# Kernel tuning notes

Measured on AMD Instinct MI355X. Metric: run time of the kernel, lower is better.

## Reference

```python
import jax, jax.numpy as jnp
import numpy as np

EPS = 1e-5
GROUPS = 8


def setup_inputs() -> dict:
    key = jax.random.key(0)
    ks = jax.random.split(key, 7)
    B, C, H, W = 4, 512, 64, 64
    x = jax.random.normal(ks[0], (B, C, H, W), dtype=jnp.float32)
    gn_w = jax.random.normal(ks[1], (C,), dtype=jnp.float32) * 0.02 + 1.0
    gn_b = jax.random.normal(ks[2], (C,), dtype=jnp.float32) * 0.02
    # 1x1 convs stored as [out, in] matrices
    qkv_w = jax.random.normal(ks[3], (3 * C, C), dtype=jnp.float32) * (C ** -0.5)
    qkv_b = jax.random.normal(ks[4], (3 * C,), dtype=jnp.float32) * 0.02
    proj_w = jax.random.normal(ks[5], (C, C), dtype=jnp.float32) * (C ** -0.5)
    proj_b = jax.random.normal(ks[6], (C,), dtype=jnp.float32) * 0.02
    return {"x": x, "gn_w": gn_w, "gn_b": gn_b, "qkv_w": qkv_w,
            "qkv_b": qkv_b, "proj_w": proj_w, "proj_b": proj_b}


def _group_norm(x, w, b):
    B, C, H, W = x.shape
    xg = x.reshape(B, GROUPS, C // GROUPS, H, W)
    mu = jnp.mean(xg, axis=(2, 3, 4), keepdims=True)
    var = jnp.var(xg, axis=(2, 3, 4), keepdims=True)
    xn = ((xg - mu) * jax.lax.rsqrt(var + EPS)).reshape(B, C, H, W)
    return xn * w[None, :, None, None] + b[None, :, None, None]


def reference(x, gn_w, gn_b, qkv_w, qkv_b, proj_w, proj_b):
    B, C, H, W = x.shape
    N = H * W
    scale = C ** (-0.5)
    h = _group_norm(x, gn_w, gn_b)
    # 1x1 conv -> [B, 3C, N]
    qkv = jnp.einsum('oc,bcn->bon', qkv_w, h.reshape(B, C, N)) + qkv_b[None, :, None]
    q, k, v = jnp.split(qkv, 3, axis=1)  # each [B, C, N]
    # scores[b, n, m] = sum_c q[b,c,n] * k[b,c,m]
    attn = jax.nn.softmax(jnp.einsum('bcn,bcm->bnm', q, k) * scale, axis=-1)
    # out[b,c,n] = sum_m v[b,c,m] * attn[b,n,m]   (v @ attn^T)
    hout = jnp.einsum('bcm,bnm->bcn', v, attn)
    proj = jnp.einsum('oc,bcn->bon', proj_w, hout) + proj_b[None, :, None]
    return x + proj.reshape(B, C, H, W)
```

## Files before the change

kernel.cpp:

```cpp
#include <hip/hip_runtime.h>
#include <math.h>

#define SCALE 0.044194173824159216f
#define QI 28.22222222f
#define K8SCL ((4.5f/127.0f)*(4.5f/127.0f)*SCALE)
#define PSCL 0.49609375f
#define VSCL 0.035433070866141736f

typedef __bf16 bf16x8 __attribute__((ext_vector_type(8)));
typedef float  f32x4  __attribute__((ext_vector_type(4)));
typedef int    i32x4  __attribute__((ext_vector_type(4)));
typedef unsigned int u32;

__device__ __forceinline__ void gload16(const void* g, void* l) {
    __builtin_amdgcn_global_load_lds(
        (const __attribute__((address_space(1))) u32*)g,
        (__attribute__((address_space(3))) u32*)l, 16, 0, 0);
}

__global__ __launch_bounds__(256) void gn_part(const float* __restrict__ x,
                                               float* __restrict__ part) {
    int gi = blockIdx.x >> 4, sl = blockIdx.x & 15;
    const float4* p = (const float4*)(x + (size_t)gi * 64 * 4096) + (size_t)sl * 4096;
    float s = 0.f, ss = 0.f;
    #pragma unroll 4
    for (int i = threadIdx.x; i < 4096; i += 256) {
        float4 v = p[i];
        s  += v.x + v.y + v.z + v.w;
        ss += v.x*v.x + v.y*v.y + v.z*v.z + v.w*v.w;
    }
    __shared__ float rs[256], rss[256];
    rs[threadIdx.x] = s; rss[threadIdx.x] = ss;
    __syncthreads();
    for (int o = 128; o > 0; o >>= 1) {
        if (threadIdx.x < o) { rs[threadIdx.x] += rs[threadIdx.x+o]; rss[threadIdx.x] += rss[threadIdx.x+o]; }
        __syncthreads();
    }
    if (threadIdx.x == 0) {
        part[blockIdx.x*2 + 0] = rs[0];
        part[blockIdx.x*2 + 1] = rss[0];
    }
}

__global__ __launch_bounds__(64) void gn_fin(const float* __restrict__ part,
                                             float* __restrict__ stats) {
    int t = threadIdx.x;
    if (t < 32) {
        float s = 0.f, ss = 0.f;
        #pragma unroll
        for (int i = 0; i < 16; ++i) { s += part[(t*16+i)*2]; ss += part[(t*16+i)*2+1]; }
        float inv = 1.0f / (float)(64 * 4096);
        float mu  = s * inv;
        float var = ss * inv - mu * mu;
        stats[t*2 + 0] = mu;
        stats[t*2 + 1] = rsqrtf(var + 1e-5f);
    }
}

__global__ __launch_bounds__(256) void gn_apply_t(const float* __restrict__ x,
                                                  const float* __restrict__ stats,
                                                  const float* __restrict__ gw,
                                                  const float* __restrict__ gb,
                                                  __bf16* __restrict__ hT) {
    __shared__ __bf16 tile[64][88];
    int b = blockIdx.z, c0 = blockIdx.y * 64, n0 = blockIdx.x * 64;
    int t = threadIdx.x;
    float mu  = stats[(b*8 + blockIdx.y)*2];
    float rsg = stats[(b*8 + blockIdx.y)*2 + 1];
    int c = t >> 2, ns = t & 3;
    float a = gw[c0+c] * rsg;
    float d = gb[c0+c] - mu * a;
    const float* xr = x + ((size_t)b*512 + c0 + c)*4096 + n0 + ns*16;
    #pragma unroll
    for (int e4 = 0; e4 < 4; ++e4) {
        float4 v = *(const float4*)(xr + e4*4);
        tile[ns*16 + e4*4 + 0][c] = (__bf16)(v.x*a + d);
        tile[ns*16 + e4*4 + 1][c] = (__bf16)(v.y*a + d);
        tile[ns*16 + e4*4 + 2][c] = (__bf16)(v.z*a + d);
        tile[ns*16 + e4*4 + 3][c] = (__bf16)(v.w*a + d);
    }
    __syncthreads();
    int n = t >> 2, cs = t & 3;
    __bf16* dst = hT + ((size_t)b*4096 + n0 + n)*512 + c0 + cs*16;
    *(uint4*)(dst)     = *(const uint4*)(&tile[n][cs*16]);
    *(uint4*)(dst + 8) = *(const uint4*)(&tile[n][cs*16 + 8]);
}

__global__ __launch_bounds__(256) void wconv2(const float* __restrict__ qw,
                                              const float* __restrict__ pwsrc,
                                              __bf16* __restrict__ dst) {
    int i = (blockIdx.x*256 + threadIdx.x) * 4;
    const float* src = (i < 786432) ? (qw + i) : (pwsrc + (i - 786432));
    float4 v = *(const float4*)src;
    dst[i+0] = (__bf16)v.x; dst[i+1] = (__bf16)v.y;
    dst[i+2] = (__bf16)v.z; dst[i+3] = (__bf16)v.w;
}

template<int MODE>
__global__ __launch_bounds__(256) void mm128(
        const __bf16* __restrict__ A, int lda, size_t sA,
        const __bf16* __restrict__ B, int ldb, size_t sB,
        int Kdim,
        const float* __restrict__ bias,
        const float* __restrict__ res, size_t sR,
        void* __restrict__ out, int ldo, size_t sO) {
    __shared__ __bf16 As[3][128][32];
    __shared__ __bf16 Bs[3][128][32];

    const int t = threadIdx.x, w = t >> 6, l = t & 63;
    const int l15 = l & 15, lq = l >> 4;
    const int bz = blockIdx.z;

    const int gx = gridDim.x;
    int lin = blockIdx.y * gx + blockIdx.x;
    {
        const int nwg = gx * gridDim.y;
        const int qn = nwg >> 3, rn = nwg & 7;
        const int xcd = lin & 7, idx = lin >> 3;
        const int base = (xcd < rn) ? xcd*(qn+1) : rn*(qn+1) + (xcd-rn)*qn;
        lin = base + idx;
    }
    const int j0 = (lin % gx) * 128;
    const int i0 = (lin / gx) * 128;

    const __bf16* Ab = A + sA*bz;
    const __bf16* Bb = B + sB*bz;
    const int rowblk = (w & 1)*64;
    const int colblk = (w >> 1)*64;

    const int slot0 = w*64 + l;
    const int rowS0 = slot0 >> 2;
    const int rowS1 = rowS0 + 64;
    const int csS   = (((slot0 & 3) ^ ((rowS0 >> 1) & 3))) * 8;
    const int off0  = (w*64)*16;
    const int off1  = (256 + w*64)*16;

    f32x4 acc[4][4];
    #pragma unroll
    for (int mr = 0; mr < 4; ++mr)
        #pragma unroll
        for (int nr = 0; nr < 4; ++nr)
            #pragma unroll
            for (int r = 0; r < 4; ++r) acc[mr][nr][r] = 0.f;

    auto STAGE = [&](int kc, int bi) {
        char* Ad = (char*)As[bi];
        char* Bd = (char*)Bs[bi];
        gload16(Ab + (size_t)(i0 + rowS0)*lda + kc + csS, Ad + off0);
        gload16(Ab + (size_t)(i0 + rowS1)*lda + kc + csS, Ad + off1);
        gload16(Bb + (size_t)(j0 + rowS0)*ldb + kc + csS, Bd + off0);
        gload16(Bb + (size_t)(j0 + rowS1)*ldb + kc + csS, Bd + off1);
    };

    const int rsw = (l15 >> 1) & 3;
    const int koff = (lq ^ rsw) << 4;

    const int nch = Kdim >> 5;
    STAGE(0, 0);
    STAGE(32, 1);

    for (int cc = 0; cc < nch; ++cc) {
        if (cc < nch - 1) asm volatile("s_waitcnt vmcnt(4)\n\ts_barrier" ::: "memory");
        else              asm volatile("s_waitcnt vmcnt(0)\n\ts_barrier" ::: "memory");

        const char* Ac = (const char*)As[cc % 3];
        const char* Bc = (const char*)Bs[cc % 3];
        bf16x8 av[4], bv[4];
        #pragma unroll
        for (int mr = 0; mr < 4; ++mr)
            av[mr] = *(const bf16x8*)(Ac + (rowblk + mr*16 + l15)*64 + koff);
        #pragma unroll
        for (int nr = 0; nr < 4; ++nr)
            bv[nr] = *(const bf16x8*)(Bc + (colblk + nr*16 + l15)*64 + koff);
        if (cc + 2 < nch) STAGE((cc + 2)*32, (cc + 2) % 3);
        #pragma unroll
        for (int mr = 0; mr < 4; ++mr)
            #pragma unroll
            for (int nr = 0; nr < 4; ++nr)
                acc[mr][nr] = __builtin_amdgcn_mfma_f32_16x16x32_bf16(av[mr], bv[nr], acc[mr][nr], 0, 0, 0);
    }

    #pragma unroll
    for (int mr = 0; mr < 4; ++mr)
        #pragma unroll
        for (int nr = 0; nr < 4; ++nr) {
            int col = j0 + colblk + nr*16 + l15;
            #pragma unroll
            for (int r = 0; r < 4; ++r) {
                int lrow = rowblk + mr*16 + lq*4 + r;
                int gi = i0 + lrow;
                float v = acc[mr][nr][r];
                if constexpr (MODE == 1) {
                    v += bias[gi];
                    int q = __float2int_rn(v * QI);
                    q = q < -127 ? -127 : (q > 127 ? 127 : q);
                    ((char*)out)[sO*bz + (size_t)gi*ldo + col] = (char)q;
                } else {
                    v += bias[gi] + res[sR*bz + (size_t)gi*ldo + col];
                    ((float*)out)[sO*bz + (size_t)gi*ldo + col] = v;
                }
            }
        }
}

template<int M> struct AccT { using T = f32x4; };
template<> struct AccT<4> { using T = i32x4; };
template<> struct AccT<5> { using T = i32x4; };

#define LDSB (98304 + 4096)
template<int MODE>
__global__ __launch_bounds__(512) void mm256(
        const void* __restrict__ A, int ldaB, size_t sAB,
        const void* __restrict__ B, int ldbB, size_t sBB,
        int Kbytes,
        const float* __restrict__ bias,
        void* __restrict__ out, int ldo, size_t sO,
        float* __restrict__ rowpart) {
    extern __shared__ char smem[];
    char*  Abase = smem;
    char*  Bbase = smem + 49152;
    float* redp  = (float*)(smem + 98304);

    const int t = threadIdx.x, w = t >> 6, l = t & 63;
    const int l15 = l & 15, lq = l >> 4;
    const int bz = (MODE == 4) ? (blockIdx.z >> 1) : blockIdx.z;
    const int kh = (MODE == 4) ? (blockIdx.z & 1) : 0;
    const size_t kbase = (size_t)kh * Kbytes;

    const int gx = gridDim.x;
    int lin = blockIdx.y * gx + blockIdx.x;
    {
        const int nwg = gx * gridDim.y;
        const int qn = nwg >> 3, rn = nwg & 7;
        const int xcd = lin & 7, idx = lin >> 3;
        const int base = (xcd < rn) ? xcd*(qn+1) : rn*(qn+1) + (xcd-rn)*qn;
        lin = base + idx;
    }
    const int j0 = (lin % gx) * 256;
    const int i0 = (lin / gx) * 256;

    const char* Ab = (const char*)A + sAB*bz + kbase;
    const char* Bb = (const char*)B + sBB*bz + kbase;
    const int wr = w & 1;
    const int wc = w >> 1;

    const int slot0 = w*64 + l;
    const int rowS0 = slot0 >> 2;
    const int rowS1 = rowS0 + 128;
    const int csS   = (((slot0 & 3) ^ ((rowS0 >> 1) & 3))) * 16;
    const int off0  = (w*64)*16;
    const int off1  = (512 + w*64)*16;

    typename AccT<MODE>::T acc[8][4];
    #pragma unroll
    for (int mr = 0; mr < 8; ++mr)
        #pragma unroll
        for (int nr = 0; nr < 4; ++nr)
            #pragma unroll
            for (int r = 0; r < 4; ++r) acc[mr][nr][r] = 0;

    auto STAGE = [&](int kc, int bi) {
        char* Ad = Abase + bi*16384;
        char* Bd = Bbase + bi*16384;
        gload16(Ab + (size_t)(i0 + rowS0)*ldaB + kc + csS, Ad + off0);
        gload16(Ab + (size_t)(i0 + rowS1)*ldaB + kc + csS, Ad + off1);
        gload16(Bb + (size_t)(j0 + rowS0)*ldbB + kc + csS, Bd + off0);
        gload16(Bb + (size_t)(j0 + rowS1)*ldbB + kc + csS, Bd + off1);
    };

    const int rsw = (l15 >> 1) & 3;
    const int koff = (lq ^ rsw) << 4;

    const int nch = Kbytes >> 6;
    STAGE(0, 0);
    STAGE(64, 1);

    for (int cc = 0; cc < nch; ++cc) {
        if (cc < nch - 1) asm volatile("s_waitcnt vmcnt(4)\n\ts_barrier" ::: "memory");
        else              asm volatile("s_waitcnt vmcnt(0)\n\ts_barrier" ::: "memory");

        const char* Ac = Abase + (cc % 3)*16384;
        const char* Bc = Bbase + (cc % 3)*16384;
        i32x4 araw[8], braw[4];
        #pragma unroll
        for (int mr = 0; mr < 8; ++mr)
            araw[mr] = *(const i32x4*)(Ac + (wr*128 + mr*16 + l15)*64 + koff);
        #pragma unroll
        for (int nr = 0; nr < 4; ++nr)
            braw[nr] = *(const i32x4*)(Bc + (wc*64 + nr*16 + l15)*64 + koff);
        if (cc + 2 < nch) STAGE((cc + 2)*64, (cc + 2) % 3);
        #pragma unroll
        for (int mr = 0; mr < 8; ++mr)
            #pragma unroll
            for (int nr = 0; nr < 4; ++nr) {
                if constexpr (MODE == 4 || MODE == 5) {
                    acc[mr][nr] = __builtin_amdgcn_mfma_i32_16x16x64_i8(
                        araw[mr], braw[nr], acc[mr][nr], 0, 0, 0);
                } else {
                    acc[mr][nr] = __builtin_amdgcn_mfma_f32_16x16x32_bf16(
                        __builtin_bit_cast(bf16x8, araw[mr]),
                        __builtin_bit_cast(bf16x8, braw[nr]), acc[mr][nr], 0, 0, 0);
                }
            }
    }

    if constexpr (MODE == 5) {
        const int jblk = j0 >> 8;
        float rpart[8][4];
        #pragma unroll
        for (int mr = 0; mr < 8; ++mr)
            #pragma unroll
            for (int r = 0; r < 4; ++r) rpart[mr][r] = 0.f;
        #pragma unroll
        for (int mr = 0; mr < 8; ++mr)
            #pragma unroll
            for (int nr = 0; nr < 4; ++nr) {
                int col = j0 + wc*64 + nr*16 + l15;
                #pragma unroll
                for (int r = 0; r < 4; ++r) {
                    int row = wr*128 + mr*16 + lq*4 + r;
                    float e = __expf((float)acc[mr][nr][r] * K8SCL);
                    int q = __float2int_rn(e * PSCL);
                    if (q > 127) q = 127;
                    ((char*)out)[sO*bz + (size_t)(i0 + row)*ldo + col] = (char)q;
                    rpart[mr][r] += (float)q;
                }
            }
        #pragma unroll
        for (int m = 1; m < 16; m <<= 1)
            #pragma unroll
            for (int mr = 0; mr < 8; ++mr)
                #pragma unroll
                for (int r = 0; r < 4; ++r)
                    rpart[mr][r] += __shfl_xor(rpart[mr][r], m);
        __syncthreads();
        if (l15 == 0) {
            #pragma unroll
            for (int mr = 0; mr < 8; ++mr)
                #pragma unroll
                for (int r = 0; r < 4; ++r)
                    redp[(wr*128 + mr*16 + lq*4 + r)*4 + wc] = rpart[mr][r];
        }
        __syncthreads();
        if (t < 256)
            rowpart[(size_t)bz*131072 + (size_t)jblk*4096 + i0 + t] =
                redp[t*4+0] + redp[t*4+1] + redp[t*4+2] + redp[t*4+3];
        return;
    }

    #pragma unroll
    for (int mr = 0; mr < 8; ++mr)
        #pragma unroll
        for (int nr = 0; nr < 4; ++nr) {
            int col = j0 + wc*64 + nr*16 + l15;
            #pragma unroll
            for (int r = 0; r < 4; ++r) {
                int lrow = wr*128 + mr*16 + lq*4 + r;
                if constexpr (MODE == 0) {
                    float v = (float)acc[mr][nr][r] + bias[col];
                    int q = __float2int_rn(v * QI);
                    q = q < -127 ? -127 : (q > 127 ? 127 : q);
                    char* qk = (char*)out + (size_t)bz*8388608;
                    size_t row = (size_t)(i0 + lrow);
                    char* p = (col < 512) ? (qk + row*512 + col)
                                          : (qk + 2097152 + row*512 + (col - 512));
                    *p = (char)q;
                } else {
                    int* po = (int*)out + sO*bz + (size_t)kh*4096*ldo;
                    po[(size_t)(i0 + lrow)*ldo + col] = acc[mr][nr][r];
                }
            }
        }
}

__global__ __launch_bounds__(256) void pv_reduce(const int* __restrict__ part,
                                                 const float* __restrict__ rowpart,
                                                 __bf16* __restrict__ OT) {
    int b = blockIdx.y, r0 = blockIdx.x * 16;
    __shared__ float rs[16];
    int t = threadIdx.x;
    if (t < 16) {
        const float* rp = rowpart + (size_t)b*131072 + r0 + t;
        float s = 0.f;
        #pragma unroll
        for (int jb = 0; jb < 16; ++jb) s += rp[jb*4096];
        rs[t] = VSCL / s;
    }
    __syncthreads();
    int row = r0 + (t >> 4), cseg = (t & 15) * 32;
    const int* p0 = part + (size_t)b*8388608 + (size_t)row*512 + cseg;
    const int* p1 = p0 + 2097152;
    __bf16* o = OT + (size_t)b*2097152 + (size_t)row*512 + cseg;
    float sc = rs[t >> 4];
    #pragma unroll
    for (int g = 0; g < 4; ++g) {
        int4 a0 = *(const int4*)(p0 + g*8);
        int4 a1 = *(const int4*)(p0 + g*8 + 4);
        int4 b0 = *(const int4*)(p1 + g*8);
        int4 b1 = *(const int4*)(p1 + g*8 + 4);
        bf16x8 r;
        r[0] = (__bf16)((float)(a0.x + b0.x) * sc);
        r[1] = (__bf16)((float)(a0.y + b0.y) * sc);
        r[2] = (__bf16)((float)(a0.z + b0.z) * sc);
        r[3] = (__bf16)((float)(a0.w + b0.w) * sc);
        r[4] = (__bf16)((float)(a1.x + b1.x) * sc);
        r[5] = (__bf16)((float)(a1.y + b1.y) * sc);
        r[6] = (__bf16)((float)(a1.z + b1.z) * sc);
        r[7] = (__bf16)((float)(a1.w + b1.w) * sc);
        *(bf16x8*)(o + g*8) = r;
    }
}

extern "C" void kernel_launch(void* const* d_in, const int* in_sizes, int n_in,
                              void* d_out, int out_size, void* d_ws, size_t ws_size,
                              hipStream_t stream) {
    const float* x      = (const float*)d_in[0];
    const float* gn_w   = (const float*)d_in[1];
    const float* gn_b   = (const float*)d_in[2];
    const float* qkv_w  = (const float*)d_in[3];
    const float* qkv_b  = (const float*)d_in[4];
    const float* proj_w = (const float*)d_in[5];
    const float* proj_b = (const float*)d_in[6];

    char* w8 = (char*)d_ws;
    char*   v8buf = w8 + 33554432;
    __bf16* OT   = (__bf16*)(w8 + 50331648);
    __bf16* wq   = (__bf16*)(w8 + 67108864);
    __bf16* pw   = (__bf16*)(w8 + 68681728);
    float*  rowpart = (float*)(w8 + 69206016);
    float*  part = (float*)(w8 + 71303168);
    float*  st   = (float*)(w8 + 71307264);
    const size_t baseP = 71307520ULL;
    __bf16* hT   = (__bf16*)(w8 + baseP);

    size_t avail = (ws_size > baseP) ? (ws_size - baseP) : 0;
    int cap = (int)(avail / 33554432ULL);
    if (cap < 1) cap = 1;
    if (cap > 4) cap = 4;

    hipFuncSetAttribute((const void*)mm256<0>,
                        hipFuncAttributeMaxDynamicSharedMemorySize, LDSB);
    hipFuncSetAttribute((const void*)mm256<4>,
                        hipFuncAttributeMaxDynamicSharedMemorySize, LDSB);
    hipFuncSetAttribute((const void*)mm256<5>,
                        hipFuncAttributeMaxDynamicSharedMemorySize, LDSB);

    wconv2<<<1024, 256, 0, stream>>>(qkv_w, proj_w, wq);
    gn_part<<<512, 256, 0, stream>>>(x, part);
    gn_fin<<<1, 64, 0, stream>>>(part, st);
    gn_apply_t<<<dim3(64, 8, 4), 256, 0, stream>>>(x, st, gn_w, gn_b, hT);

    mm256<0><<<dim3(4, 16, 4), 512, LDSB, stream>>>(
        hT, 1024, (size_t)4096*1024, wq, 1024, 0, 1024,
        qkv_b, w8, 0, 0, nullptr);
    mm128<1><<<dim3(32, 4, 4), 256, 0, stream>>>(
        wq + (size_t)1024*512, 512, 0, hT, 512, (size_t)4096*512, 512,
        qkv_b + 1024, nullptr, 0, v8buf, 4096, (size_t)512*4096);

    for (int b0 = 0; b0 < 4; b0 += cap) {
        int c = (4 - b0 < cap) ? (4 - b0) : cap;
        char* Pb = w8 + baseP + (size_t)b0*33554432;
        mm256<5><<<dim3(16, 16, c), 512, LDSB, stream>>>(
            w8 + (size_t)b0*8388608, 512, 8388608,
            w8 + (size_t)b0*8388608 + 2097152, 512, 8388608, 512,
            nullptr, Pb, 4096, 33554432,
            rowpart + (size_t)b0*131072);
        mm256<4><<<dim3(2, 16, c*2), 512, LDSB, stream>>>(
            Pb, 4096, 33554432,
            v8buf + (size_t)b0*2097152, 4096, 2097152, 2048,
            nullptr, Pb + 16777216, 512, 8388608,
            nullptr);
        pv_reduce<<<dim3(256, c), 256, 0, stream>>>(
            (const int*)(Pb + 16777216), rowpart + (size_t)b0*131072,
            OT + (size_t)b0*2097152);
    }

    mm128<2><<<dim3(32, 4, 4), 256, 0, stream>>>(
        pw, 512, 0, OT, 512, (size_t)4096*512, 512,
        proj_b, x, (size_t)512*4096, (float*)d_out, 4096, (size_t)512*4096);
}
```

Baseline: 202.9 us.

## Stage GEMM epilogues through LDS, store split-K partials as bf16, fuse weight conversion

The QK-softmax (MODE 5) and QKV (MODE 0) epilogues of the 256-tile GEMM now write quantized int8 results into an LDS tile first. Each row is then written out with 16-byte coalesced stores instead of scattered byte stores. The split-K PV partials are stored as bf16 rather than int32, which halves partial traffic into pv_reduce but rounds large integer accumulators. The weight-conversion kernel is also folded into the GroupNorm partial-sum launch, and exp is rewritten as exp2 with a pre-folded constant.

```diff
diff --git a/kernel.cpp b/kernel.cpp
--- a/kernel.cpp
+++ b/kernel.cpp
@@ -4,6 +4,7 @@
 #define SCALE 0.044194173824159216f
 #define QI 28.22222222f
 #define K8SCL ((4.5f/127.0f)*(4.5f/127.0f)*SCALE)
+#define K8SCL2 (K8SCL * 1.4426950408889634f)
 #define PSCL 0.49609375f
 #define VSCL 0.035433070866141736f
 
@@ -18,8 +19,22 @@
         (__attribute__((address_space(3))) u32*)l, 16, 0, 0);
 }
 
-__global__ __launch_bounds__(256) void gn_part(const float* __restrict__ x,
-                                               float* __restrict__ part) {
+__global__ __launch_bounds__(256) void gn_part_w(const float* __restrict__ x,
+                                                 float* __restrict__ part,
+                                                 const float* __restrict__ qw,
+                                                 const float* __restrict__ pwsrc,
+                                                 __bf16* __restrict__ wdst) {
+    if (blockIdx.x >= 512) {
+        int i = ((blockIdx.x - 512)*256 + threadIdx.x) * 4;
+        #pragma unroll
+        for (int rep = 0; rep < 4; ++rep, i += 262144) {
+            const float* src = (i < 786432) ? (qw + i) : (pwsrc + (i - 786432));
+            float4 v = *(const float4*)src;
+            wdst[i+0] = (__bf16)v.x; wdst[i+1] = (__bf16)v.y;
+            wdst[i+2] = (__bf16)v.z; wdst[i+3] = (__bf16)v.w;
+        }
+        return;
+    }
     int gi = blockIdx.x >> 4, sl = blockIdx.x & 15;
     const float4* p = (const float4*)(x + (size_t)gi * 64 * 4096) + (size_t)sl * 4096;
     float s = 0.f, ss = 0.f;
@@ -86,16 +101,6 @@
     *(uint4*)(dst + 8) = *(const uint4*)(&tile[n][cs*16 + 8]);
 }
 
-__global__ __launch_bounds__(256) void wconv2(const float* __restrict__ qw,
-                                              const float* __restrict__ pwsrc,
-                                              __bf16* __restrict__ dst) {
-    int i = (blockIdx.x*256 + threadIdx.x) * 4;
-    const float* src = (i < 786432) ? (qw + i) : (pwsrc + (i - 786432));
-    float4 v = *(const float4*)src;
-    dst[i+0] = (__bf16)v.x; dst[i+1] = (__bf16)v.y;
-    dst[i+2] = (__bf16)v.z; dst[i+3] = (__bf16)v.w;
-}
-
 template<int MODE>
 __global__ __launch_bounds__(256) void mm128(
         const __bf16* __restrict__ A, int lda, size_t sA,
@@ -220,6 +225,7 @@
     char*  Abase = smem;
     char*  Bbase = smem + 49152;
     float* redp  = (float*)(smem + 98304);
+    char*  ptile = smem;
 
     const int t = threadIdx.x, w = t >> 6, l = t & 63;
     const int l15 = l & 15, lq = l >> 4;
@@ -311,18 +317,19 @@
         for (int mr = 0; mr < 8; ++mr)
             #pragma unroll
             for (int r = 0; r < 4; ++r) rpart[mr][r] = 0.f;
+        __syncthreads();
         #pragma unroll
         for (int mr = 0; mr < 8; ++mr)
             #pragma unroll
             for (int nr = 0; nr < 4; ++nr) {
-                int col = j0 + wc*64 + nr*16 + l15;
+                int colL = wc*64 + nr*16 + l15;
                 #pragma unroll
                 for (int r = 0; r < 4; ++r) {
                     int row = wr*128 + mr*16 + lq*4 + r;
-                    float e = __expf((float)acc[mr][nr][r] * K8SCL);
+                    float e = exp2f((float)acc[mr][nr][r] * K8SCL2);
                     int q = __float2int_rn(e * PSCL);
                     if (q > 127) q = 127;
-                    ((char*)out)[sO*bz + (size_t)(i0 + row)*ldo + col] = (char)q;
+                    ptile[row*272 + colL] = (char)q;
                     rpart[mr][r] += (float)q;
                 }
             }
@@ -333,7 +340,6 @@
                 #pragma unroll
                 for (int r = 0; r < 4; ++r)
                     rpart[mr][r] += __shfl_xor(rpart[mr][r], m);
-        __syncthreads();
         if (l15 == 0) {
             #pragma unroll
             for (int mr = 0; mr < 8; ++mr)
@@ -342,12 +348,50 @@
                     redp[(wr*128 + mr*16 + lq*4 + r)*4 + wc] = rpart[mr][r];
         }
         __syncthreads();
+        {
+            int row = t >> 1, half = t & 1;
+            const char* src = ptile + row*272 + half*128;
+            char* dst = (char*)out + sO*bz + (size_t)(i0 + row)*ldo + j0 + half*128;
+            #pragma unroll
+            for (int i = 0; i < 8; ++i)
+                *(uint4*)(dst + i*16) = *(const uint4*)(src + i*16);
+        }
         if (t < 256)
             rowpart[(size_t)bz*131072 + (size_t)jblk*4096 + i0 + t] =
                 redp[t*4+0] + redp[t*4+1] + redp[t*4+2] + redp[t*4+3];
         return;
     }
 
+    if constexpr (MODE == 0) {
+        __syncthreads();
+        #pragma unroll
+        for (int mr = 0; mr < 8; ++mr)
+            #pragma unroll
+            for (int nr = 0; nr < 4; ++nr) {
+                int colL = wc*64 + nr*16 + l15;
+                float b = bias[j0 + colL];
+                #pragma unroll
+                for (int r = 0; r < 4; ++r) {
+                    int row = wr*128 + mr*16 + lq*4 + r;
+                    float v = (float)acc[mr][nr][r] + b;
+                    int q = __float2int_rn(v * QI);
+                    q = q < -127 ? -127 : (q > 127 ? 127 : q);
+                    ptile[row*272 + colL] = (char)q;
+                }
+            }
+        __syncthreads();
+        int row = t >> 1, half = t & 1;
+        int colg = j0 + half*128;
+        const char* src = ptile + row*272 + half*128;
+        char* qk = (char*)out + (size_t)bz*8388608;
+        char* dst = (colg < 512) ? (qk + (size_t)(i0 + row)*512 + colg)
+                                 : (qk + 2097152 + (size_t)(i0 + row)*512 + (colg - 512));
+        #pragma unroll
+        for (int i = 0; i < 8; ++i)
+            *(uint4*)(dst + i*16) = *(const uint4*)(src + i*16);
+        return;
+    }
+
     #pragma unroll
     for (int mr = 0; mr < 8; ++mr)
         #pragma unroll
@@ -356,24 +400,13 @@
             #pragma unroll
             for (int r = 0; r < 4; ++r) {
                 int lrow = wr*128 + mr*16 + lq*4 + r;
-                if constexpr (MODE == 0) {
-                    float v = (float)acc[mr][nr][r] + bias[col];
-                    int q = __float2int_rn(v * QI);
-                    q = q < -127 ? -127 : (q > 127 ? 127 : q);
-                    char* qk = (char*)out + (size_t)bz*8388608;
-                    size_t row = (size_t)(i0 + lrow);
-                    char* p = (col < 512) ? (qk + row*512 + col)
-                                          : (qk + 2097152 + row*512 + (col - 512));
-                    *p = (char)q;
-                } else {
-                    int* po = (int*)out + sO*bz + (size_t)kh*4096*ldo;
-                    po[(size_t)(i0 + lrow)*ldo + col] = acc[mr][nr][r];
-                }
+                __bf16* po = (__bf16*)out + sO*bz + (size_t)kh*2097152;
+                po[(size_t)(i0 + lrow)*ldo + col] = (__bf16)(float)acc[mr][nr][r];
             }
         }
 }
 
-__global__ __launch_bounds__(256) void pv_reduce(const int* __restrict__ part,
+__global__ __launch_bounds__(256) void pv_reduce(const __bf16* __restrict__ part,
                                                  const float* __restrict__ rowpart,
                                                  __bf16* __restrict__ OT) {
     int b = blockIdx.y, r0 = blockIdx.x * 16;
@@ -388,25 +421,17 @@
     }
     __syncthreads();
     int row = r0 + (t >> 4), cseg = (t & 15) * 32;
-    const int* p0 = part + (size_t)b*8388608 + (size_t)row*512 + cseg;
-    const int* p1 = p0 + 2097152;
+    const __bf16* p0 = part + (size_t)b*16777216 + (size_t)row*512 + cseg;
+    const __bf16* p1 = p0 + 2097152;
     __bf16* o = OT + (size_t)b*2097152 + (size_t)row*512 + cseg;
     float sc = rs[t >> 4];
     #pragma unroll
     for (int g = 0; g < 4; ++g) {
-        int4 a0 = *(const int4*)(p0 + g*8);
-        int4 a1 = *(const int4*)(p0 + g*8 + 4);
-        int4 b0 = *(const int4*)(p1 + g*8);
-        int4 b1 = *(const int4*)(p1 + g*8 + 4);
+        bf16x8 a = *(const bf16x8*)(p0 + g*8);
+        bf16x8 bb = *(const bf16x8*)(p1 + g*8);
         bf16x8 r;
-        r[0] = (__bf16)((float)(a0.x + b0.x) * sc);
-        r[1] = (__bf16)((float)(a0.y + b0.y) * sc);
-        r[2] = (__bf16)((float)(a0.z + b0.z) * sc);
-        r[3] = (__bf16)((float)(a0.w + b0.w) * sc);
-        r[4] = (__bf16)((float)(a1.x + b1.x) * sc);
-        r[5] = (__bf16)((float)(a1.y + b1.y) * sc);
-        r[6] = (__bf16)((float)(a1.z + b1.z) * sc);
-        r[7] = (__bf16)((float)(a1.w + b1.w) * sc);
+        #pragma unroll
+        for (int e = 0; e < 8; ++e) r[e] = (__bf16)(((float)a[e] + (float)bb[e]) * sc);
         *(bf16x8*)(o + g*8) = r;
     }
 }
@@ -445,8 +470,7 @@
     hipFuncSetAttribute((const void*)mm256<5>,
                         hipFuncAttributeMaxDynamicSharedMemorySize, LDSB);
 
-    wconv2<<<1024, 256, 0, stream>>>(qkv_w, proj_w, wq);
-    gn_part<<<512, 256, 0, stream>>>(x, part);
+    gn_part_w<<<768, 256, 0, stream>>>(x, part, qkv_w, proj_w, wq);
     gn_fin<<<1, 64, 0, stream>>>(part, st);
     gn_apply_t<<<dim3(64, 8, 4), 256, 0, stream>>>(x, st, gn_w, gn_b, hT);
 
@@ -468,10 +492,10 @@
         mm256<4><<<dim3(2, 16, c*2), 512, LDSB, stream>>>(
             Pb, 4096, 33554432,
             v8buf + (size_t)b0*2097152, 4096, 2097152, 2048,
-            nullptr, Pb + 16777216, 512, 8388608,
+            nullptr, Pb + 16777216, 512, 16777216,
             nullptr);
         pv_reduce<<<dim3(256, c), 256, 0, stream>>>(
-            (const int*)(Pb + 16777216), rowpart + (size_t)b0*131072,
+            (const __bf16*)(Pb + 16777216), rowpart + (size_t)b0*131072,
             OT + (size_t)b0*2097152);
     }
 
```

Result: slower. 219.1 us (+8.0%).
